# Kernel tuning notes

Hardware: AMD Instinct MI355X
Metric: run time of the kernel (lower is better)

The kernel has to match this reference:

```python
import jax, jax.numpy as jnp
import numpy as np
import math

B, NO, T, NM, P = 16, 64, 21, 768, 20
CA, CM, D, H, L, K = 29, 9, 256, 8, 6, 16
N = NO + NM
HD = D // H


def _linrelu(x, w, b):
    return jax.nn.relu(x @ w.T + b)


def _layernorm(x, g, b):
    m = x.mean(-1, keepdims=True)
    v = ((x - m) ** 2).mean(-1, keepdims=True)
    return (x - m) / jnp.sqrt(v + 1e-5) * g + b


def _sine_embed(pos_xy, d):
    # MTR gen_sineembed_for_position: per-coordinate sin/cos, concat(y, x)
    half = d // 2
    dim_t = 10000.0 ** (2.0 * (jnp.arange(half) // 2).astype(jnp.float32) / half)
    scale = 2.0 * math.pi
    def interleave(e):
        return jnp.stack([jnp.sin(e[..., 0::2]), jnp.cos(e[..., 1::2])], axis=-1).reshape(e.shape)
    ex = pos_xy[..., 0:1] * scale / dim_t
    ey = pos_xy[..., 1:2] * scale / dim_t
    return jnp.concatenate([interleave(ey), interleave(ex)], axis=-1)


def _pointnet(poly, mask, pre, mid, out1, out2):
    # PointNetPolylineEncoder: pre-MLP, masked max-pool, concat pooled, MLP, masked max-pool, out-MLP
    m = mask[..., None].astype(poly.dtype)
    f = poly
    for w, b in pre:
        f = _linrelu(f, w, b)
    f = f * m  # zero invalid points (== scatter into zeros)
    pooled = f.max(axis=2)
    f = jnp.concatenate([f, jnp.broadcast_to(pooled[:, :, None, :], f.shape)], axis=-1)
    for w, b in mid:
        f = _linrelu(f, w, b)
    f = f * m
    f = f.max(axis=2)  # [B, num_poly, hidden]
    h = _linrelu(f, out1[0], out1[1])
    h = h @ out2[0].T + out2[1]
    valid = mask.any(-1)
    return jnp.where(valid[..., None], h, 0.0)


def _forward(obj_trajs, map_polylines, obj_trajs_last_pos, map_polylines_center,
             a_pre_w, a_pre_b, a_mlp_w1, a_mlp_b1, a_mlp_w2, a_mlp_b2,
             a_out_w1, a_out_b1, a_out_w2, a_out_b2,
             m_pre_w1, m_pre_b1, m_pre_w2, m_pre_b2, m_pre_w3, m_pre_b3,
             m_mlp_w1, m_mlp_b1, m_mlp_w2, m_mlp_b2,
             m_out_w1, m_out_b1, m_out_w2, m_out_b2,
             attn_wqkv, attn_bqkv, attn_wo, attn_bo,
             ffn_w1, ffn_b1, ffn_w2, ffn_b2,
             ln1_g, ln1_b, ln2_g, ln2_b,
             obj_trajs_mask, map_polylines_mask):
    obj_in = jnp.concatenate([obj_trajs, obj_trajs_mask[..., None].astype(obj_trajs.dtype)], axis=-1)
    obj_feat = _pointnet(obj_in, obj_trajs_mask, [(a_pre_w, a_pre_b)],
                         [(a_mlp_w1, a_mlp_b1), (a_mlp_w2, a_mlp_b2)],
                         (a_out_w1, a_out_b1), (a_out_w2, a_out_b2))
    map_feat = _pointnet(map_polylines, map_polylines_mask,
                         [(m_pre_w1, m_pre_b1), (m_pre_w2, m_pre_b2), (m_pre_w3, m_pre_b3)],
                         [(m_mlp_w1, m_mlp_b1), (m_mlp_w2, m_mlp_b2)],
                         (m_out_w1, m_out_b1), (m_out_w2, m_out_b2))
    x = jnp.concatenate([obj_feat, map_feat], axis=1)                      # [B, N, D]
    pos = jnp.concatenate([obj_trajs_last_pos, map_polylines_center], axis=1)  # [B, N, 3]
    # KNN neighbor graph within each batch element (all tokens valid)
    d2 = jnp.sum((pos[:, :, None, :] - pos[:, None, :, :]) ** 2, axis=-1)  # [B, N, N]
    _, idx = jax.lax.top_k(-d2, K)                                          # [B, N, K]
    pe = _sine_embed(pos[..., :2], D)                                       # [B, N, D]
    scaling = HD ** -0.5
    gather = jax.vmap(lambda a, i: a[i])  # per-batch neighbor gather
    out = x
    for l in range(L):  # post-norm transformer encoder layers with local (KNN) attention
        qk_in = out + pe
        wq, wk, wv = attn_wqkv[l, :D], attn_wqkv[l, D:2 * D], attn_wqkv[l, 2 * D:]
        bq, bk, bv = attn_bqkv[l, :D], attn_bqkv[l, D:2 * D], attn_bqkv[l, 2 * D:]
        q = ((qk_in @ wq.T + bq) * scaling).reshape(B, N, H, HD)
        k = (qk_in @ wk.T + bk).reshape(B, N, H, HD)
        v = (out @ wv.T + bv).reshape(B, N, H, HD)
        kg = gather(k, idx)  # [B, N, K, H, HD]
        vg = gather(v, idx)
        attn = jax.nn.softmax(jnp.einsum('bnhd,bnkhd->bnhk', q, kg), axis=-1)
        o = jnp.einsum('bnhk,bnkhd->bnhd', attn, vg).reshape(B, N, D)
        o = o @ attn_wo[l].T + attn_bo[l]
        h = _layernorm(out + o, ln1_g[l], ln1_b[l])
        ff = jax.nn.relu(h @ ffn_w1[l].T + ffn_b1[l]) @ ffn_w2[l].T + ffn_b2[l]
        out = _layernorm(h + ff, ln2_g[l], ln2_b[l])
    return out  # global_token_feature [B, N, D]


def setup_inputs():
    ks = iter(jax.random.split(jax.random.key(0), 64))
    def rn(shape, s=1.0):
        return jax.random.normal(next(ks), shape, dtype=jnp.float32) * s
    w = 0.02
    inp = {
        'obj_trajs': rn((B, NO, T, CA)),
        'map_polylines': rn((B, NM, P, CM)),
        'obj_trajs_last_pos': rn((B, NO, 3)),
        'map_polylines_center': rn((B, NM, 3)),
        'a_pre_w': rn((D, CA + 1), w), 'a_pre_b': rn((D,), w),
        'a_mlp_w1': rn((D, 2 * D), w), 'a_mlp_b1': rn((D,), w),
        'a_mlp_w2': rn((D, D), w), 'a_mlp_b2': rn((D,), w),
        'a_out_w1': rn((D, D), w), 'a_out_b1': rn((D,), w),
        'a_out_w2': rn((D, D), w), 'a_out_b2': rn((D,), w),
        'm_pre_w1': rn((64, CM), w), 'm_pre_b1': rn((64,), w),
        'm_pre_w2': rn((64, 64), w), 'm_pre_b2': rn((64,), w),
        'm_pre_w3': rn((64, 64), w), 'm_pre_b3': rn((64,), w),
        'm_mlp_w1': rn((64, 128), w), 'm_mlp_b1': rn((64,), w),
        'm_mlp_w2': rn((64, 64), w), 'm_mlp_b2': rn((64,), w),
        'm_out_w1': rn((64, 64), w), 'm_out_b1': rn((64,), w),
        'm_out_w2': rn((D, 64), w), 'm_out_b2': rn((D,), w),
        'attn_wqkv': rn((L, 3 * D, D), w), 'attn_bqkv': rn((L, 3 * D), w),
        'attn_wo': rn((L, D, D), w), 'attn_bo': rn((L, D), w),
        'ffn_w1': rn((L, 4 * D, D), w), 'ffn_b1': rn((L, 4 * D), w),
        'ffn_w2': rn((L, D, 4 * D), w), 'ffn_b2': rn((L, D), w),
        'ln1_g': jnp.ones((L, D), jnp.float32), 'ln1_b': jnp.zeros((L, D), jnp.float32),
        'ln2_g': jnp.ones((L, D), jnp.float32), 'ln2_b': jnp.zeros((L, D), jnp.float32),
        'obj_trajs_mask': jnp.ones((B, NO, T), bool),
        'map_polylines_mask': jnp.ones((B, NM, P), bool),
        'track_index_to_predict': jax.random.randint(next(ks), (B,), 0, NO),
    }
    return inp


def reference(obj_trajs, map_polylines, obj_trajs_last_pos, map_polylines_center,
              a_pre_w, a_pre_b, a_mlp_w1, a_mlp_b1, a_mlp_w2, a_mlp_b2,
              a_out_w1, a_out_b1, a_out_w2, a_out_b2,
              m_pre_w1, m_pre_b1, m_pre_w2, m_pre_b2, m_pre_w3, m_pre_b3,
              m_mlp_w1, m_mlp_b1, m_mlp_w2, m_mlp_b2,
              m_out_w1, m_out_b1, m_out_w2, m_out_b2,
              attn_wqkv, attn_bqkv, attn_wo, attn_bo,
              ffn_w1, ffn_b1, ffn_w2, ffn_b2,
              ln1_g, ln1_b, ln2_g, ln2_b,
              obj_trajs_mask, map_polylines_mask, track_index_to_predict):
    # track_index_to_predict only selects rows of the output downstream; core encoder output returned
    return _forward(obj_trajs, map_polylines, obj_trajs_last_pos, map_polylines_center,
                    a_pre_w, a_pre_b, a_mlp_w1, a_mlp_b1, a_mlp_w2, a_mlp_b2,
                    a_out_w1, a_out_b1, a_out_w2, a_out_b2,
                    m_pre_w1, m_pre_b1, m_pre_w2, m_pre_b2, m_pre_w3, m_pre_b3,
                    m_mlp_w1, m_mlp_b1, m_mlp_w2, m_mlp_b2,
                    m_out_w1, m_out_b1, m_out_w2, m_out_b2,
                    attn_wqkv, attn_bqkv, attn_wo, attn_bo,
                    ffn_w1, ffn_b1, ffn_w2, ffn_b2,
                    ln1_g, ln1_b, ln2_g, ln2_b,
                    obj_trajs_mask, map_polylines_mask)
```

## Files before the change

kernel.cpp:

```cpp
#include <hip/hip_runtime.h>
#include <hip/hip_bf16.h>

typedef unsigned short u16;
typedef _Float16 h16;

#define BB 16
#define NO 64
#define TT 21
#define NM 768
#define PP 20
#define CAx 29
#define CMx 9
#define DD 256
#define HH 8
#define LL 6
#define KK 16
#define NN (NO + NM)
#define HDX (DD / HH)
#define MTOT (BB * NN)
#define MAPR (BB * NM * PP)

typedef __attribute__((ext_vector_type(8))) h16 h8v;
typedef __attribute__((ext_vector_type(4))) h16 h4v;
typedef __attribute__((ext_vector_type(4))) float f4v;
// ... 209 lines not shown
                GLOAD_LDS16(&W[(size_t)(n0 + r + lrow) * K + k0 + lcol], &WS[r][0]);
            }
        }
        __syncthreads();
        h8v af[WM];
        #pragma unroll
        for (int mi = 0; mi < WM; mi++)
            af[mi] = *(const h8v*)&AS[wr * (WM * 16) + mi * 16 + fr][rdo];
        #pragma unroll
        for (int nj = 0; nj < 4; nj++) {
            h8v bf = *(const h8v*)&WS[wc * 64 + nj * 16 + fr][rdo];
            #pragma unroll
            for (int mi = 0; mi < WM; mi++)
                acc[mi][nj] = __builtin_amdgcn_mfma_f32_16x16x32_f16(af[mi], bf, acc[mi][nj], 0, 0, 0);
        }
    }
    #pragma unroll
    for (int mi = 0; mi < WM; mi++) {
        #pragma unroll
        for (int nj = 0; nj < 4; nj++) {
            int col = n0 + wc * 64 + nj * 16 + fr;
            float bb = bias ? bias[col] : 0.f;
            #pragma unroll
            for (int r = 0; r < 4; r++) {
                int row = m0 + wr * (WM * 16) + mi * 16 + (lane >> 4) * 4 + r;
                float v = acc[mi][nj][r] + bb;
                if (addrow) v += addrow[(size_t)(row / ardiv) * arld + col];
                if (RELU) v = fmaxf(v, 0.f);
                if (F16OUT) {
                    C16[(size_t)row * ldc + col] = (h16)v;
                } else {
                    int drow = row;
                    if (ROWMAP) drow = row + rm_add + (row / rm_div) * rm_mul;
                    Cf[(size_t)drow * ldc + col] = v;
                }
            }
        }
    }
}

__global__ __launch_bounds__(256) void split_x0(
    const float* __restrict__ X, const h16* __restrict__ PE16,
    h16* __restrict__ X16, h16* __restrict__ XP16)
{
    size_t base = ((size_t)blockIdx.x * 256 + threadIdx.x) * 4;
    float4 x = *(const float4*)&X[base];
    h4v pe = *(const h4v*)&PE16[base];
    h4v a, b;
    a.x = (h16)x.x; a.y = (h16)x.y; a.z = (h16)x.z; a.w = (h16)x.w;
    b.x = (h16)(x.x + (float)pe.x); b.y = (h16)(x.y + (float)pe.y);
    b.z = (h16)(x.z + (float)pe.z); b.w = (h16)(x.w + (float)pe.w);
    *(h4v*)&X16[base] = a;
    *(h4v*)&XP16[base] = b;
}

__global__ __launch_bounds__(256) void fused_map3(
    const h16* __restrict__ A,
    const h16* __restrict__ W1,
    const h16* __restrict__ W2, const h16* __restrict__ W3,
    const float* __restrict__ b1, const float* __restrict__ b2, const float* __restrict__ b3,
    h16* __restrict__ Out)
{
    __shared__ __align__(16) h16 AS[128][32];
    __shared__ __align__(16) h16 G0[2][128][32];
    __shared__ __align__(16) h16 G1[2][128][32];
    __shared__ __align__(16) h16 W1S[64][32];
    __shared__ __align__(16) h16 W2S[2][64][32];
    __shared__ __align__(16) h16 W3S[2][64][32];
    const int m0 = blockIdx.x * 128;
    const int tid = threadIdx.x;
    const int wave = tid >> 6, lane = tid & 63;
    const int fr = lane & 15, kb = lane >> 4;
    const int lrow = lane >> 2, lcol = SWZ_LCOL(lane);
    const int rdo = SWZ_RD(kb, fr);

    #pragma unroll
    for (int q = 0; q < 2; q++)
        GLOAD_LDS16(&A[(size_t)(m0 + wave * 32 + q * 16 + lrow) * 32 + lcol],
                    &AS[wave * 32 + q * 16][0]);
    GLOAD_LDS16(&W1[(size_t)(wave * 16 + lrow) * 32 + lcol], &W1S[wave * 16][0]);
    #pragma unroll
    for (int t = 0; t < 2; t++) {
        GLOAD_LDS16(&W2[(size_t)(wave * 16 + lrow) * 64 + t * 32 + lcol], &W2S[t][wave * 16][0]);
        GLOAD_LDS16(&W3[(size_t)(wave * 16 + lrow) * 64 + t * 32 + lcol], &W3S[t][wave * 16][0]);
    }
    __syncthreads();
    #pragma unroll
    for (int mi = 0; mi < 2; mi++) {
        h8v af = *(const h8v*)&AS[wave * 32 + mi * 16 + fr][rdo];
        #pragma unroll
        for (int nj = 0; nj < 4; nj++) {
            f4v a = {0.f, 0.f, 0.f, 0.f};
            h8v bf = *(const h8v*)&W1S[nj * 16 + fr][rdo];
            a = __builtin_amdgcn_mfma_f32_16x16x32_f16(af, bf, a, 0, 0, 0);
            int col = nj * 16 + fr, ch = col >> 5, kl = col & 31;
            float bb = b1[col];
            #pragma unroll
            for (int r = 0; r < 4; r++) {
                int row = wave * 32 + mi * 16 + kb * 4 + r;
                G0[ch][row][SWZ_ELEM(row, kl)] = (h16)fmaxf(a[r] + bb, 0.f);
            }
        }
    }
    __syncthreads();
    #pragma unroll
    for (int mi = 0; mi < 2; mi++) {
        #pragma unroll
        for (int nj = 0; nj < 4; nj++) {
            f4v a = {0.f, 0.f, 0.f, 0.f};
            #pragma unroll
            for (int t = 0; t < 2; t++) {
                h8v af = *(const h8v*)&G0[t][wave * 32 + mi * 16 + fr][rdo];
                h8v bf = *(const h8v*)&W2S[t][nj * 16 + fr][rdo];
                a = __builtin_amdgcn_mfma_f32_16x16x32_f16(af, bf, a, 0, 0, 0);
            }
            int col = nj * 16 + fr, ch = col >> 5, kl = col & 31;
            float bb = b2[col];
            #pragma unroll
            for (int r = 0; r < 4; r++) {
                int row = wave * 32 + mi * 16 + kb * 4 + r;
                G1[ch][row][SWZ_ELEM(row, kl)] = (h16)fmaxf(a[r] + bb, 0.f);
            }
        }
    }
    __syncthreads();
    #pragma unroll
    for (int mi = 0; mi < 2; mi++) {
        #pragma unroll
        for (int nj = 0; nj < 4; nj++) {
            f4v a = {0.f, 0.f, 0.f, 0.f};
            #pragma unroll
            for (int t = 0; t < 2; t++) {
                h8v af = *(const h8v*)&G1[t][wave * 32 + mi * 16 + fr][rdo];
                h8v bf = *(const h8v*)&W3S[t][nj * 16 + fr][rdo];
                a = __builtin_amdgcn_mfma_f32_16x16x32_f16(af, bf, a, 0, 0, 0);
            }
            int col = nj * 16 + fr;
            float bb = b3[col];
            #pragma unroll
            for (int r = 0; r < 4; r++) {
                int row = m0 + wave * 32 + mi * 16 + kb * 4 + r;
                Out[(size_t)row * 64 + col] = (h16)fmaxf(a[r] + bb, 0.f);
            }
        }
    }
}

__global__ __launch_bounds__(256) void fused_map2(
    const h16* __restrict__ A,
    const h16* __restrict__ W1,
    const h16* __restrict__ W2,
    const float* __restrict__ b2,
    const float* __restrict__ pooled,
    h16* __restrict__ Out)
{
    __shared__ __align__(16) h16 AS[2][128][32];
    __shared__ __align__(16) h16 G0[2][128][32];
    __shared__ __align__(16) h16 W1S[2][64][32];
    __shared__ __align__(16) h16 W2S[2][64][32];
    const int m0 = blockIdx.x * 128;
    const int tid = threadIdx.x;
    const int wave = tid >> 6, lane = tid & 63;
    const int fr = lane & 15, kb = lane >> 4;
    const int lrow = lane >> 2, lcol = SWZ_LCOL(lane);
    const int rdo = SWZ_RD(kb, fr);

    #pragma unroll
    for (int t = 0; t < 2; t++) {
        #pragma unroll
        for (int q = 0; q < 2; q++)
            GLOAD_LDS16(&A[(size_t)(m0 + wave * 32 + q * 16 + lrow) * 64 + t * 32 + lcol],
                        &AS[t][wave * 32 + q * 16][0]);
        GLOAD_LDS16(&W1[(size_t)(wave * 16 + lrow) * 64 + t * 32 + lcol], &W1S[t][wave * 16][0]);
        GLOAD_LDS16(&W2[(size_t)(wave * 16 + lrow) * 64 + t * 32 + lcol], &W2S[t][wave * 16][0]);
    }
    __syncthreads();
    #pragma unroll
    for (int mi = 0; mi < 2; mi++) {
        #pragma unroll
        for (int nj = 0; nj < 4; nj++) {
            f4v a = {0.f, 0.f, 0.f, 0.f};
            #pragma unroll
            for (int t = 0; t < 2; t++) {
                h8v af = *(const h8v*)&AS[t][wave * 32 + mi * 16 + fr][rdo];
                h8v bf = *(const h8v*)&W1S[t][nj * 16 + fr][rdo];
                a = __builtin_amdgcn_mfma_f32_16x16x32_f16(af, bf, a, 0, 0, 0);
            }
            int col = nj * 16 + fr, ch = col >> 5, kl = col & 31;
            #pragma unroll
            for (int r = 0; r < 4; r++) {
                int row = wave * 32 + mi * 16 + kb * 4 + r;
                int grow = m0 + row;
                float v = a[r] + pooled[(size_t)(grow / PP) * 64 + col];
                G0[ch][row][SWZ_ELEM(row, kl)] = (h16)fmaxf(v, 0.f);
            }
        }
    }
    __syncthreads();
    #pragma unroll
    for (int mi = 0; mi < 2; mi++) {
        #pragma unroll
        for (int nj = 0; nj < 4; nj++) {
            f4v a = {0.f, 0.f, 0.f, 0.f};
            #pragma unroll
            for (int t = 0; t < 2; t++) {
                h8v af = *(const h8v*)&G0[t][wave * 32 + mi * 16 + fr][rdo];
                h8v bf = *(const h8v*)&W2S[t][nj * 16 + fr][rdo];
                a = __builtin_amdgcn_mfma_f32_16x16x32_f16(af, bf, a, 0, 0, 0);
            }
            int col = nj * 16 + fr;
            float bb = b2[col];
            #pragma unroll
            for (int r = 0; r < 4; r++) {
                int row = m0 + wave * 32 + mi * 16 + kb * 4 + r;
                Out[(size_t)row * 64 + col] = (h16)fmaxf(a[r] + bb, 0.f);
            }
        }
    }
}

template<bool RELU, bool F16OUT>
__global__ __launch_bounds__(256) void gemm_mfma(
    const h16* __restrict__ A, const h16* __restrict__ A2, int a2min,
    const h16* __restrict__ W, const float* __restrict__ bias,
    float* __restrict__ Cf, h16* __restrict__ C16,
    int K, int ldc, int coff, float scale, int scale_until)
{
    __shared__ __align__(16) h16 AS[128][32];
    __shared__ __align__(16) h16 WS[128][32];
    const int m0 = blockIdx.x * 128;
    const int n0 = blockIdx.y * 128;
    const h16* pA = (n0 >= a2min) ? A2 : A;
    const int tid = threadIdx.x;
    const int wave = tid >> 6, lane = tid & 63;
    const int wr = wave >> 1, wc = wave & 1;
    const int fr = lane & 15, kb = lane >> 4;
    const int lrow = lane >> 2;
    const int lcol = SWZ_LCOL(lane);
    const int rdo = SWZ_RD(kb, fr);

    f4v acc[4][4];
    #pragma unroll
    for (int i = 0; i < 4; i++)
        #pragma unroll
        for (int j = 0; j < 4; j++) { f4v z = {0.f, 0.f, 0.f, 0.f}; acc[i][j] = z; }

    for (int k0 = 0; k0 < K; k0 += 32) {
        __syncthreads();
        #pragma unroll
        for (int i = 0; i < 2; i++) {
            const int r = wave * 32 + i * 16;
            const size_t grow = (size_t)(r + lrow);
            GLOAD_LDS16(&pA[(m0 + grow) * K + k0 + lcol], &AS[r][0]);
            GLOAD_LDS16(&W [(n0 + grow) * K + k0 + lcol], &WS[r][0]);
        }
        __syncthreads();
        h8v af[4];
        #pragma unroll
        for (int mi = 0; mi < 4; mi++)
            af[mi] = *(const h8v*)&AS[wr * 64 + mi * 16 + fr][rdo];
        #pragma unroll
        for (int nj = 0; nj < 4; nj++) {
            h8v bf = *(const h8v*)&WS[wc * 64 + nj * 16 + fr][rdo];
            #pragma unroll
            for (int mi = 0; mi < 4; mi++)
                acc[mi][nj] = __builtin_amdgcn_mfma_f32_16x16x32_f16(af[mi], bf, acc[mi][nj], 0, 0, 0);
        }
    }
    #pragma unroll
    for (int mi = 0; mi < 4; mi++) {
        #pragma unroll
        for (int nj = 0; nj < 4; nj++) {
            int col = n0 + wc * 64 + nj * 16 + fr;
            float bb = bias[col];
            #pragma unroll
            for (int r = 0; r < 4; r++) {
                int row = m0 + wr * 64 + mi * 16 + (lane >> 4) * 4 + r;
                float v = acc[mi][nj][r] + bb;
                if (RELU) v = fmaxf(v, 0.f);
                int gcol = coff + col;
                if (gcol < scale_until) v *= scale;
                if (F16OUT) {
                    C16[(size_t)row * ldc + gcol] = (h16)v;
                } else {
                    Cf[(size_t)row * ldc + gcol] = v;
                }
            }
        }
    }
}

template<int PEMODE>
__global__ __launch_bounds__(512) void fused_layer(
    const h16* __restrict__ AO16, const h16* __restrict__ Wo,
    const float* __restrict__ bo, const h16* __restrict__ X16r,
    const float* __restrict__ g1, const float* __restrict__ bt1,
    const h16* __restrict__ W1,
    const h16* __restrict__ W2,
    const float* __restrict__ b1, const float* __restrict__ b2,
    const float* __restrict__ g2, const float* __restrict__ bt2,
    float* __restrict__ OutF, h16* __restrict__ O16,
    const h16* __restrict__ PE16p, h16* __restrict__ P16)
{
    __shared__ __align__(16) h16 AOS[8][32][32];
    __shared__ __align__(16) h16 HS[8][32][32];
    __shared__ __align__(16) h16 GS[2][32][32];
    __shared__ __align__(16) h16 WSu[16384];
    __shared__ float red_s[2][8][32];
    const int m0 = blockIdx.x * 32;
    const int tid = threadIdx.x;
    const int wave = tid >> 6, lane = tid & 63;
    const int fr = lane & 15, kb = lane >> 4;
    const int lrow = lane >> 2, lcol = SWZ_LCOL(lane);
    const int rdo = SWZ_RD(kb, fr);
    const int mi1 = wave >> 2, nj1 = wave & 3;

    #pragma unroll
    for (int q = 0; q < 2; q++)
        GLOAD_LDS16(&AO16[(size_t)(m0 + q * 16 + lrow) * 256 + wave * 32 + lcol],
                    &AOS[wave][q * 16][0]);

    float xo[4][4];
    float rsum1[4] = {0.f, 0.f, 0.f, 0.f}, rsq1[4] = {0.f, 0.f, 0.f, 0.f};
    #pragma unroll
    for (int oc = 0; oc < 4; oc++) {
        __syncthreads();
        #pragma unroll
        for (int q = 0; q < 4; q++)
            GLOAD_LDS16(&Wo[(size_t)(oc * 64 + q * 16 + lrow) * 256 + wave * 32 + lcol],
                        &WSu[wave * 2048 + (q * 16) * 32]);
        __syncthreads();
        f4v o1 = {0.f, 0.f, 0.f, 0.f};
        #pragma unroll
        for (int t = 0; t < 8; t++) {
            h8v af = *(const h8v*)&AOS[t][mi1 * 16 + fr][rdo];
            h8v bf = *(const h8v*)&WSu[t * 2048 + (nj1 * 16 + fr) * 32 + rdo];
            o1 = __builtin_amdgcn_mfma_f32_16x16x32_f16(af, bf, o1, 0, 0, 0);
        }
        int col = oc * 64 + nj1 * 16 + fr;
        float bb = bo[col];
        #pragma unroll
        for (int r = 0; r < 4; r++) {
            int row = mi1 * 16 + kb * 4 + r;
            float v = o1[r] + bb + (float)X16r[(size_t)(m0 + row) * 256 + col];
            xo[oc][r] = v;
            rsum1[r] += v;
            rsq1[r] += v * v;
        }
    }
    #pragma unroll
    for (int off = 1; off < 16; off <<= 1)
        #pragma unroll
        for (int r = 0; r < 4; r++) {
            rsum1[r] += __shfl_xor(rsum1[r], off);
            rsq1[r]  += __shfl_xor(rsq1[r], off);
        }
    if (fr == 0) {
        #pragma unroll
        for (int r = 0; r < 4; r++) {
            red_s[0][wave][mi1 * 16 + kb * 4 + r] = rsum1[r];
            red_s[1][wave][mi1 * 16 + kb * 4 + r] = rsq1[r];
        }
    } else if (fr == 1) {
        #pragma unroll
        for (int r = 0; r < 4; r++) {
            red_s[0][wave][(1 - mi1) * 16 + kb * 4 + r] = 0.f;
            red_s[1][wave][(1 - mi1) * 16 + kb * 4 + r] = 0.f;
        }
    }
    __syncthreads();
    float mean1[4], inv1[4];
    #pragma unroll
    for (int r = 0; r < 4; r++) {
        int rid = mi1 * 16 + kb * 4 + r;
        float s = 0.f, sq = 0.f;
        #pragma unroll
        for (int w = 0; w < 8; w++) { s += red_s[0][w][rid]; sq += red_s[1][w][rid]; }
        mean1[r] = s * (1.f / 256.f);
        float var = sq * (1.f / 256.f) - mean1[r] * mean1[r];
        inv1[r] = rsqrtf(var + 1e-5f);
    }
    #pragma unroll
    for (int oc = 0; oc < 4; oc++) {
        int col = oc * 64 + nj1 * 16 + fr;
        int ch = col >> 5, kl = col & 31;
        float gg = g1[col], bb = bt1[col];
        #pragma unroll
        for (int r = 0; r < 4; r++) {
            int row = mi1 * 16 + kb * 4 + r;
            float h = (xo[oc][r] - mean1[r]) * inv1[r] * gg + bb;
            HS[ch][row][SWZ_ELEM(row, kl)] = (h16)h;
        }
    }
    __syncthreads();

    f4v acc2[2][2];
    #pragma unroll
    for (int i = 0; i < 2; i++)
        #pragma unroll
        for (int j = 0; j < 2; j++) { f4v z = {0.f, 0.f, 0.f, 0.f}; acc2[i][j] = z; }

    for (int c = 0; c < 16; c++) {
        const int H0 = c * 64;
        __syncthreads();
        #pragma unroll
        for (int q = 0; q < 4; q++)
            GLOAD_LDS16(&W1[(size_t)(H0 + q * 16 + lrow) * 256 + wave * 32 + lcol],
                        &WSu[wave * 2048 + (q * 16) * 32]);
        __syncthreads();
        f4v a1 = {0.f, 0.f, 0.f, 0.f};
        #pragma unroll
        for (int t = 0; t < 8; t++) {
            h8v af = *(const h8v*)&HS[t][mi1 * 16 + fr][rdo];
            h8v bf = *(const h8v*)&WSu[t * 2048 + (nj1 * 16 + fr) * 32 + rdo];
            a1 = __builtin_amdgcn_mfma_f32_16x16x32_f16(af, bf, a1, 0, 0, 0);
        }
        {
            int col = nj1 * 16 + fr, ch = col >> 5, kl = col & 31;
            float bb = b1[H0 + col];
            #pragma unroll
            for (int r = 0; r < 4; r++) {
                int row = mi1 * 16 + kb * 4 + r;
                GS[ch][row][SWZ_ELEM(row, kl)] = (h16)fmaxf(a1[r] + bb, 0.f);
            }
        }
        __syncthreads();
        #pragma unroll
        for (int t2 = 0; t2 < 2; t2++)
            #pragma unroll
            for (int q = 0; q < 2; q++)
                GLOAD_LDS16(&W2[(size_t)(wave * 32 + q * 16 + lrow) * 1024 + H0 + t2 * 32 + lcol],
                            &WSu[t2 * 8192 + (wave * 32 + q * 16) * 32]);
        __syncthreads();
        #pragma unroll
        for (int t2 = 0; t2 < 2; t2++) {
            #pragma unroll
            for (int mi = 0; mi < 2; mi++) {
                h8v af = *(const h8v*)&GS[t2][mi * 16 + fr][rdo];
                #pragma unroll
                for (int nj = 0; nj < 2; nj++) {
                    h8v bf = *(const h8v*)&WSu[t2 * 8192 + (wave * 32 + nj * 16 + fr) * 32 + rdo];
                    acc2[mi][nj] = __builtin_amdgcn_mfma_f32_16x16x32_f16(af, bf, acc2[mi][nj], 0, 0, 0);
                }
            }
        }
    }
    float x[2][2][4];
    float rsum[2][4], rsq[2][4];
    #pragma unroll
    for (int mi = 0; mi < 2; mi++)
        #pragma unroll
        for (int r = 0; r < 4; r++) { rsum[mi][r] = 0.f; rsq[mi][r] = 0.f; }
    #pragma unroll
    for (int mi = 0; mi < 2; mi++) {
        #pragma unroll
        for (int nj = 0; nj < 2; nj++) {
            int col = wave * 32 + nj * 16 + fr;
            int ch = col >> 5, kl = col & 31;
            float bb = b2[col];
            #pragma unroll
            for (int r = 0; r < 4; r++) {
                int row = mi * 16 + kb * 4 + r;
                float res = (float)HS[ch][row][SWZ_ELEM(row, kl)];
                float v = acc2[mi][nj][r] + bb + res;
                x[mi][nj][r] = v;
                rsum[mi][r] += v;
                rsq[mi][r] += v * v;
            }
        }
    }
    #pragma unroll
    for (int off = 1; off < 16; off <<= 1) {
        #pragma unroll
        for (int mi = 0; mi < 2; mi++)
            #pragma unroll
            for (int r = 0; r < 4; r++) {
                rsum[mi][r] += __shfl_xor(rsum[mi][r], off);
                rsq[mi][r]  += __shfl_xor(rsq[mi][r], off);
            }
    }
    __syncthreads();
    if (fr == 0) {
        #pragma unroll
        for (int mi = 0; mi < 2; mi++)
            #pragma unroll
            for (int r = 0; r < 4; r++) {
                int rid = mi * 16 + kb * 4 + r;
                red_s[0][wave][rid] = rsum[mi][r];
                red_s[1][wave][rid] = rsq[mi][r];
            }
    }
    __syncthreads();
    #pragma unroll
    for (int mi = 0; mi < 2; mi++) {
        #pragma unroll
        for (int r = 0; r < 4; r++) {
            int rid = mi * 16 + kb * 4 + r;
            float s = 0.f, sq = 0.f;
            #pragma unroll
            for (int w = 0; w < 8; w++) { s += red_s[0][w][rid]; sq += red_s[1][w][rid]; }
            float mean = s * (1.f / 256.f);
            float var = sq * (1.f / 256.f) - mean * mean;
            float inv = rsqrtf(var + 1e-5f);
            #pragma unroll
            for (int nj = 0; nj < 2; nj++) {
                int col = wave * 32 + nj * 16 + fr;
                float o = (x[mi][nj][r] - mean) * inv * g2[col] + bt2[col];
                size_t idx = (size_t)(m0 + rid) * 256 + col;
                if (PEMODE == 2) {
                    OutF[idx] = o;
                } else {
                    O16[idx] = (h16)o;
                    P16[idx] = (h16)(o + (float)PE16p[idx]);
                }
            }
        }
    }
}

__global__ __launch_bounds__(256) void attn_kernel(
    const h16* __restrict__ QKV16, const int* __restrict__ IDX,
    h16* __restrict__ AO16)
{
    __shared__ __align__(16) h16 Ks[32][256];
    __shared__ float p_s[2][HH][16];
    __shared__ int gid_s[2][16];
    const int sub = threadIdx.x >> 7;
    const int t = threadIdx.x & 127;
    const int wave = threadIdx.x >> 6, lane = threadIdx.x & 63;
    const int xcd = blockIdx.x & 7;
    const int j = blockIdx.x >> 3;
    const int b = (j / 416) * 8 + xcd;
    const int row = b * NN + (j % 416) * 2 + sub;
    const int h = t >> 4, k = t & 15;
    int nb = IDX[(size_t)row * 16 + k];
    int g = b * NN + nb;
    if (h == 0) gid_s[sub][k] = g;
    __syncthreads();
    #pragma unroll
    for (int i = 0; i < 4; i++) {
        int s0 = wave * 8 + i * 2;
        int s = s0 + (lane >> 5);
        int gs = gid_s[s >> 4][s & 15];
        int clog = (lane & 31) ^ (s & 7);
        GLOAD_LDS16(&QKV16[(size_t)gs * 768 + 256 + clog * 8], &Ks[s0][0]);
    }
    __syncthreads();
    const h16* q = &QKV16[(size_t)row * 768 + h * HDX];
    const int sidx = sub * 16 + k;
    float s = 0.f;
    #pragma unroll
    for (int c = 0; c < 4; c++) {
        h8v q8 = *(const h8v*)&q[c * 8];
        h8v k8 = *(const h8v*)&Ks[sidx][(((h * 4 + c) ^ (sidx & 7)) * 8)];
        #pragma unroll
        for (int e = 0; e < 8; e++) s += (float)q8[e] * (float)k8[e];
    }
    float m = s;
    #pragma unroll
    for (int off = 8; off; off >>= 1) m = fmaxf(m, __shfl_xor(m, off, 16));
    float e = expf(s - m);
    float sum = e;
    #pragma unroll
    for (int off = 8; off; off >>= 1) sum += __shfl_xor(sum, off, 16);
    p_s[sub][h][k] = e / sum;
    __syncthreads();
    const int d0 = t * 2;
    const int hh = d0 >> 5, dd = d0 & 31;
    float o0 = 0.f, o1 = 0.f;
    #pragma unroll
    for (int kk = 0; kk < 16; kk++) {
        int gg = gid_s[sub][kk];
        const h16* vr = &QKV16[(size_t)gg * 768 + 512 + hh * HDX + dd];
        float p = p_s[sub][hh][kk];
        o0 += p * (float)vr[0];
        o1 += p * (float)vr[1];
    }
    size_t base = (size_t)row * DD + d0;
    AO16[base] = (h16)o0;
    AO16[base + 1] = (h16)o1;
}

extern "C" void kernel_launch(void* const* d_in, const int* in_sizes, int n_in,
                              void* d_out, int out_size, void* d_ws, size_t ws_size,
                              hipStream_t stream)
{
    const float* obj      = (const float*)d_in[0];
    const float* mp       = (const float*)d_in[1];
    const float* opos     = (const float*)d_in[2];
    const float* mpos     = (const float*)d_in[3];
    const float* a_pre_w  = (const float*)d_in[4];
    const float* a_pre_b  = (const float*)d_in[5];
    const float* a_mlp_w1 = (const float*)d_in[6];
    const float* a_mlp_b1 = (const float*)d_in[7];
    const float* a_mlp_w2 = (const float*)d_in[8];
    const float* a_mlp_b2 = (const float*)d_in[9];
    const float* a_out_w1 = (const float*)d_in[10];
    const float* a_out_b1 = (const float*)d_in[11];
    const float* a_out_w2 = (const float*)d_in[12];
    const float* a_out_b2 = (const float*)d_in[13];
    const float* m_pre_w1 = (const float*)d_in[14];
    const float* m_pre_b1 = (const float*)d_in[15];
    const float* m_pre_w2 = (const float*)d_in[16];
    const float* m_pre_b2 = (const float*)d_in[17];
    const float* m_pre_w3 = (const float*)d_in[18];
    const float* m_pre_b3 = (const float*)d_in[19];
    const float* m_mlp_w1 = (const float*)d_in[20];
    const float* m_mlp_b1 = (const float*)d_in[21];
    const float* m_mlp_w2 = (const float*)d_in[22];
    const float* m_mlp_b2 = (const float*)d_in[23];
    const float* m_out_w1 = (const float*)d_in[24];
    const float* m_out_b1 = (const float*)d_in[25];
    const float* m_out_w2 = (const float*)d_in[26];
    const float* m_out_b2 = (const float*)d_in[27];
    const float* attn_wqkv = (const float*)d_in[28];
    const float* attn_bqkv = (const float*)d_in[29];
    const float* attn_wo   = (const float*)d_in[30];
    const float* attn_bo   = (const float*)d_in[31];
    const float* ffn_w1    = (const float*)d_in[32];
    const float* ffn_b1    = (const float*)d_in[33];
    const float* ffn_w2    = (const float*)d_in[34];
    const float* ffn_b2    = (const float*)d_in[35];
    const float* ln1_g     = (const float*)d_in[36];
    const float* ln1_b     = (const float*)d_in[37];
    const float* ln2_g     = (const float*)d_in[38];
    const float* ln2_b     = (const float*)d_in[39];

    const size_t M = MTOT;
    float* ws   = (float*)d_ws;
    float* X    = ws;
    float* PEr  = X   + M * 256;
    float* QKVr = PEr + M * 256;
    float* Hpad = QKVr + M * 768;
    h16* AO16   = (h16*)(Hpad + M * 256);
    h16* X16    = AO16 + M * 256;
    h16* XP16   = X16  + M * 256;
    h16* H16    = XP16 + M * 256;
    h16* whf    = H16  + M * 256;
    h16* wpnf   = whf  + 4718592;
    int* IDX    = (int*)(wpnf + WPN_TOT);

    h16* PE16 = (h16*)PEr;
    h16* QKV16 = (h16*)QKVr;

    h16* PN0f = (h16*)QKVr;
    h16* PN1f = PN0f + 15728640;
    h16* SB   = PN0f + 31457280;
    h16* PLf  = SB;
    h16* GMf  = SB + 786432;
    h16* HVf  = SB + 1572864;
    h16* APLf = SB + 2359296;
    h16* AGMf = SB + 2621440;
    h16* AHVf = SB + 2883584;
    float* PCf = (float*)(SB + 3145728);
    float* APC = PCf + 786432;

    knn_kernel<<<BB * 208, 256, 0, stream>>>(opos, mpos, IDX);
    prep_all<<<PRB_TOT, 256, 0, stream>>>(
        mp, obj, opos, mpos,
        attn_wqkv, attn_wo, ffn_w1, ffn_w2,
        m_pre_w1, m_pre_w2, m_pre_w3, m_mlp_w1, m_mlp_w2, m_out_w1, m_out_w2,
        a_pre_w, a_mlp_w1, a_mlp_w2, a_out_w1, a_out_w2,
        PN0f , PN1f , PE16, wpnf, whf);

    {
        h16* PA32 = PN1f;
        h16* PB   = PN0f + 7864320;
        h16* PA2  = PN1f;
        gemm_pn<128, true, true, false><<<dim3(168, 2), 256, 0, stream>>>(
            PA32, wpnf + APW_O, a_pre_b, nullptr, 1, 0,
            nullptr, PB, 32, 256, 1, 0, 0);
        pool_max8<21><<<128, 256, 0, stream>>>(PB, APLf, 8);
        gemm_pn<128, false, false, false><<<dim3(8, 2), 256, 0, stream>>>(
            APLf, wpnf + AW1B_O, a_mlp_b1, nullptr, 1, 0,
            APC, nullptr, 256, 256, 1, 0, 0);
        gemm_pn<128, true, true, false><<<dim3(168, 2), 256, 0, stream>>>(
            PB, wpnf + AW1A_O, nullptr, APC, 21, 256,
            nullptr, PA2, 256, 256, 1, 0, 0);
        gemm_pn<128, true, true, false><<<dim3(168, 2), 256, 0, stream>>>(
            PA2, wpnf + AW2S_O, a_mlp_b2, nullptr, 1, 0,
            nullptr, PB, 256, 256, 1, 0, 0);
        pool_max8<21><<<128, 256, 0, stream>>>(PB, AGMf, 8);
        gemm_pn<128, true, true, false><<<dim3(8, 2), 256, 0, stream>>>(
            AGMf, wpnf + AOW1_O, a_out_b1, nullptr, 1, 0,
            nullptr, AHVf, 256, 256, 1, 0, 0);
        gemm_pn<128, false, false, true><<<dim3(8, 2), 256, 0, stream>>>(
            AHVf, wpnf + AOW2_O, a_out_b2, nullptr, 1, 0,
            X, nullptr, 256, 256, 64, 768, 0);
    }

    {
        fused_map3<<<MAPR / 128, 256, 0, stream>>>(
            PN0f, wpnf + W1P_O, wpnf + W2S_O, wpnf + W3S_O,
            m_pre_b1, m_pre_b2, m_pre_b3, PN1f);
        pool_max8<20><<<384, 256, 0, stream>>>(PN1f, PLf, 6);
        gemm_pn<64, false, false, false><<<dim3(96, 1), 256, 0, stream>>>(
            PLf, wpnf + MW1B_O, m_mlp_b1, nullptr, 1, 0,
            PCf, nullptr, 64, 64, 1, 0, 0);
        fused_map2<<<MAPR / 128, 256, 0, stream>>>(
            PN1f, wpnf + MW1A_O, wpnf + MW2S_O,
            m_mlp_b2, PCf, PN0f);
        pool_max8<20><<<384, 256, 0, stream>>>(PN0f, GMf, 6);
        gemm_pn<64, true, true, false><<<dim3(96, 1), 256, 0, stream>>>(
            GMf, wpnf + OW1S_O, m_out_b1, nullptr, 1, 0,
            nullptr, HVf, 64, 64, 1, 0, 0);
        gemm_pn<128, false, false, true><<<dim3(96, 2), 256, 0, stream>>>(
            HVf, wpnf + OW2S_O, m_out_b2, nullptr, 1, 0,
            X, nullptr, 64, 256, 768, 64, 64);
    }

    split_x0<<<(int)(M * 256 / 1024), 256, 0, stream>>>(X, PE16, X16, XP16);

    const float scal = 0.17677669529663687f;
    const int MB = MTOT / 128;
    for (int l = 0; l < LL; l++) {
        const size_t wb = (size_t)l * 786432;
        const h16* wqkv_f = whf + wb;
        const h16* wo_f   = whf + wb + 196608;
        const h16* f1_f   = whf + wb + 262144;
        const h16* f2_f   = whf + wb + 524288;
        const float* bqkv = attn_bqkv + (size_t)l * 768;
        gemm_mfma<false, true><<<dim3(MB, 6), 256, 0, stream>>>(
            XP16, X16, 512, wqkv_f, bqkv,
            nullptr, QKV16, 256, 768, 0, scal, 256);
        attn_kernel<<<MTOT / 2, 256, 0, stream>>>(QKV16, IDX, AO16);
        if (l == LL - 1) {
            fused_layer<2><<<MTOT / 32, 512, 0, stream>>>(
                AO16, wo_f, attn_bo + (size_t)l * 256, X16,
                ln1_g + l * 256, ln1_b + l * 256,
                f1_f, f2_f, ffn_b1 + (size_t)l * 1024, ffn_b2 + (size_t)l * 256,
                ln2_g + l * 256, ln2_b + l * 256,
                (float*)d_out, nullptr, nullptr, nullptr);
        } else {
            fused_layer<1><<<MTOT / 32, 512, 0, stream>>>(
                AO16, wo_f, attn_bo + (size_t)l * 256, X16,
                ln1_g + l * 256, ln1_b + l * 256,
                f1_f, f2_f, ffn_b1 + (size_t)l * 1024, ffn_b2 + (size_t)l * 256,
                ln2_g + l * 256, ln2_b + l * 256,
                nullptr, X16, PE16, XP16);
        }
    }
}
```

Measured before the change: 688.6 us.

## Double fused layer row tile to 64 and widen per-wave output tiles

The fused out-projection + LN + FFN + LN kernel now processes 64 rows per block instead of 32. Waves are rearranged into a 4x2 grid, each computing a 16-row by 64/128-column tile with A fragments held in registers. The larger tile halves how often each block reloads weight tiles (Wo, W1, W2) per row, which cuts weight traffic and barrier count per row. In exchange it uses roughly double the LDS and more registers, and launches half as many blocks, which may lower occupancy.

Result: no change. 682.0 us (-1.0%).

```diff
diff --git a/kernel.cpp b/kernel.cpp
--- a/kernel.cpp
+++ b/kernel.cpp
@@ -535,50 +535,56 @@
     float* __restrict__ OutF, h16* __restrict__ O16,
     const h16* __restrict__ PE16p, h16* __restrict__ P16)
 {
-    __shared__ __align__(16) h16 AOS[8][32][32];
-    __shared__ __align__(16) h16 HS[8][32][32];
-    __shared__ __align__(16) h16 GS[2][32][32];
-    __shared__ __align__(16) h16 WSu[16384];
-    __shared__ float red_s[2][8][32];
-    const int m0 = blockIdx.x * 32;
+    __shared__ __align__(16) h16 AOS[8][64][32];
+    __shared__ __align__(16) h16 HS[8][64][32];
+    __shared__ __align__(16) h16 GS[4][64][32];
+    __shared__ __align__(16) h16 WSu[32768];
+    __shared__ float red_s[2][8][64];
+    const int m0 = blockIdx.x * 64;
     const int tid = threadIdx.x;
     const int wave = tid >> 6, lane = tid & 63;
+    const int wr = wave >> 1, wc = wave & 1;
     const int fr = lane & 15, kb = lane >> 4;
     const int lrow = lane >> 2, lcol = SWZ_LCOL(lane);
     const int rdo = SWZ_RD(kb, fr);
-    const int mi1 = wave >> 2, nj1 = wave & 3;
-
-    #pragma unroll
-    for (int q = 0; q < 2; q++)
+
+    #pragma unroll
+    for (int q = 0; q < 4; q++)
         GLOAD_LDS16(&AO16[(size_t)(m0 + q * 16 + lrow) * 256 + wave * 32 + lcol],
                     &AOS[wave][q * 16][0]);
 
-    float xo[4][4];
+    float xo[2][4][4];
     float rsum1[4] = {0.f, 0.f, 0.f, 0.f}, rsq1[4] = {0.f, 0.f, 0.f, 0.f};
     #pragma unroll
-    for (int oc = 0; oc < 4; oc++) {
+    for (int oc = 0; oc < 2; oc++) {
         __syncthreads();
         #pragma unroll
-        for (int q = 0; q < 4; q++)
-            GLOAD_LDS16(&Wo[(size_t)(oc * 64 + q * 16 + lrow) * 256 + wave * 32 + lcol],
-                        &WSu[wave * 2048 + (q * 16) * 32]);
+        for (int q = 0; q < 8; q++)
+            GLOAD_LDS16(&Wo[(size_t)(oc * 128 + q * 16 + lrow) * 256 + wave * 32 + lcol],
+                        &WSu[wave * 4096 + (q * 16) * 32]);
         __syncthreads();
-        f4v o1 = {0.f, 0.f, 0.f, 0.f};
-        #pragma unroll
-        for (int t = 0; t < 8; t++) {
-            h8v af = *(const h8v*)&AOS[t][mi1 * 16 + fr][rdo];
-            h8v bf = *(const h8v*)&WSu[t * 2048 + (nj1 * 16 + fr) * 32 + rdo];
-            o1 = __builtin_amdgcn_mfma_f32_16x16x32_f16(af, bf, o1, 0, 0, 0);
-        }
-        int col = oc * 64 + nj1 * 16 + fr;
-        float bb = bo[col];
-        #pragma unroll
-        for (int r = 0; r < 4; r++) {
-            int row = mi1 * 16 + kb * 4 + r;
-            float v = o1[r] + bb + (float)X16r[(size_t)(m0 + row) * 256 + col];
-            xo[oc][r] = v;
-            rsum1[r] += v;
-            rsq1[r] += v * v;
+        h8v aof[8];
+        #pragma unroll
+        for (int t = 0; t < 8; t++)
+            aof[t] = *(const h8v*)&AOS[t][wr * 16 + fr][rdo];
+        #pragma unroll
+        for (int nj = 0; nj < 4; nj++) {
+            f4v o1 = {0.f, 0.f, 0.f, 0.f};
+            #pragma unroll
+            for (int t = 0; t < 8; t++) {
+                h8v bf = *(const h8v*)&WSu[t * 4096 + (wc * 64 + nj * 16 + fr) * 32 + rdo];
+                o1 = __builtin_amdgcn_mfma_f32_16x16x32_f16(aof[t], bf, o1, 0, 0, 0);
+            }
+            int col = oc * 128 + wc * 64 + nj * 16 + fr;
+            float bb = bo[col];
+            #pragma unroll
+            for (int r = 0; r < 4; r++) {
+                int row = wr * 16 + kb * 4 + r;
+                float v = o1[r] + bb + (float)X16r[(size_t)(m0 + row) * 256 + col];
+                xo[oc][nj][r] = v;
+                rsum1[r] += v;
+                rsq1[r] += v * v;
+            }
         }
     }
     #pragma unroll
@@ -588,24 +594,19 @@
             rsum1[r] += __shfl_xor(rsum1[r], off);
             rsq1[r]  += __shfl_xor(rsq1[r], off);
         }
-    if (fr == 0) {
+    if (fr < 4) {
+        int grp = (wr + fr) & 3;
         #pragma unroll
         for (int r = 0; r < 4; r++) {
-            red_s[0][wave][mi1 * 16 + kb * 4 + r] = rsum1[r];
-            red_s[1][wave][mi1 * 16 + kb * 4 + r] = rsq1[r];
-        }
-    } else if (fr == 1) {
-        #pragma unroll
-        for (int r = 0; r < 4; r++) {
-            red_s[0][wave][(1 - mi1) * 16 + kb * 4 + r] = 0.f;
-            red_s[1][wave][(1 - mi1) * 16 + kb * 4 + r] = 0.f;
+            red_s[0][wave][grp * 16 + kb * 4 + r] = (fr == 0) ? rsum1[r] : 0.f;
+            red_s[1][wave][grp * 16 + kb * 4 + r] = (fr == 0) ? rsq1[r] : 0.f;
         }
     }
     __syncthreads();
     float mean1[4], inv1[4];
     #pragma unroll
     for (int r = 0; r < 4; r++) {
-        int rid = mi1 * 16 + kb * 4 + r;
+        int rid = wr * 16 + kb * 4 + r;
         float s = 0.f, sq = 0.f;
         #pragma unroll
         for (int w = 0; w < 8; w++) { s += red_s[0][w][rid]; sq += red_s[1][w][rid]; }
@@ -614,138 +615,126 @@
         inv1[r] = rsqrtf(var + 1e-5f);
     }
     #pragma unroll
-    for (int oc = 0; oc < 4; oc++) {
-        int col = oc * 64 + nj1 * 16 + fr;
-        int ch = col >> 5, kl = col & 31;
-        float gg = g1[col], bb = bt1[col];
-        #pragma unroll
-        for (int r = 0; r < 4; r++) {
-            int row = mi1 * 16 + kb * 4 + r;
-            float h = (xo[oc][r] - mean1[r]) * inv1[r] * gg + bb;
-            HS[ch][row][SWZ_ELEM(row, kl)] = (h16)h;
-        }
-    }
-    __syncthreads();
-
-    f4v acc2[2][2];
-    #pragma unroll
-    for (int i = 0; i < 2; i++)
-        #pragma unroll
-        for (int j = 0; j < 2; j++) { f4v z = {0.f, 0.f, 0.f, 0.f}; acc2[i][j] = z; }
-
-    for (int c = 0; c < 16; c++) {
-        const int H0 = c * 64;
+    for (int oc = 0; oc < 2; oc++)
+        #pragma unroll
+        for (int nj = 0; nj < 4; nj++) {
+            int col = oc * 128 + wc * 64 + nj * 16 + fr;
+            int ch = col >> 5, kl = col & 31;
+            float gg = g1[col], bb = bt1[col];
+            #pragma unroll
+            for (int r = 0; r < 4; r++) {
+                int row = wr * 16 + kb * 4 + r;
+                float h = (xo[oc][nj][r] - mean1[r]) * inv1[r] * gg + bb;
+                HS[ch][row][SWZ_ELEM(row, kl)] = (h16)h;
+            }
+        }
+    __syncthreads();
+
+    h8v haf[8];
+    #pragma unroll
+    for (int t = 0; t < 8; t++)
+        haf[t] = *(const h8v*)&HS[t][wr * 16 + fr][rdo];
+
+    f4v acc2[8];
+    #pragma unroll
+    for (int j = 0; j < 8; j++) { f4v z = {0.f, 0.f, 0.f, 0.f}; acc2[j] = z; }
+
+    for (int c = 0; c < 8; c++) {
+        const int H0 = c * 128;
         __syncthreads();
         #pragma unroll
-        for (int q = 0; q < 4; q++)
+        for (int q = 0; q < 8; q++)
             GLOAD_LDS16(&W1[(size_t)(H0 + q * 16 + lrow) * 256 + wave * 32 + lcol],
-                        &WSu[wave * 2048 + (q * 16) * 32]);
+                        &WSu[wave * 4096 + (q * 16) * 32]);
         __syncthreads();
-        f4v a1 = {0.f, 0.f, 0.f, 0.f};
-        #pragma unroll
-        for (int t = 0; t < 8; t++) {
-            h8v af = *(const h8v*)&HS[t][mi1 * 16 + fr][rdo];
-            h8v bf = *(const h8v*)&WSu[t * 2048 + (nj1 * 16 + fr) * 32 + rdo];
-            a1 = __builtin_amdgcn_mfma_f32_16x16x32_f16(af, bf, a1, 0, 0, 0);
-        }
-        {
-            int col = nj1 * 16 + fr, ch = col >> 5, kl = col & 31;
-            float bb = b1[H0 + col];
+        #pragma unroll
+        for (int nj = 0; nj < 4; nj++) {
+            f4v a1 = {0.f, 0.f, 0.f, 0.f};
+            #pragma unroll
+            for (int t = 0; t < 8; t++) {
+                h8v bf = *(const h8v*)&WSu[t * 4096 + (wc * 64 + nj * 16 + fr) * 32 + rdo];
+                a1 = __builtin_amdgcn_mfma_f32_16x16x32_f16(haf[t], bf, a1, 0, 0, 0);
+            }
+            int n = wc * 64 + nj * 16 + fr;
+            int ch = n >> 5, kl = n & 31;
+            float bb = b1[H0 + n];
             #pragma unroll
             for (int r = 0; r < 4; r++) {
-                int row = mi1 * 16 + kb * 4 + r;
+                int row = wr * 16 + kb * 4 + r;
                 GS[ch][row][SWZ_ELEM(row, kl)] = (h16)fmaxf(a1[r] + bb, 0.f);
             }
         }
         __syncthreads();
         #pragma unroll
-        for (int t2 = 0; t2 < 2; t2++)
+        for (int t2 = 0; t2 < 4; t2++)
             #pragma unroll
             for (int q = 0; q < 2; q++)
                 GLOAD_LDS16(&W2[(size_t)(wave * 32 + q * 16 + lrow) * 1024 + H0 + t2 * 32 + lcol],
                             &WSu[t2 * 8192 + (wave * 32 + q * 16) * 32]);
         __syncthreads();
         #pragma unroll
-        for (int t2 = 0; t2 < 2; t2++) {
-            #pragma unroll
-            for (int mi = 0; mi < 2; mi++) {
-                h8v af = *(const h8v*)&GS[t2][mi * 16 + fr][rdo];
-                #pragma unroll
-                for (int nj = 0; nj < 2; nj++) {
-                    h8v bf = *(const h8v*)&WSu[t2 * 8192 + (wave * 32 + nj * 16 + fr) * 32 + rdo];
-                    acc2[mi][nj] = __builtin_amdgcn_mfma_f32_16x16x32_f16(af, bf, acc2[mi][nj], 0, 0, 0);
-                }
-            }
-        }
-    }
-    float x[2][2][4];
-    float rsum[2][4], rsq[2][4];
-    #pragma unroll
-    for (int mi = 0; mi < 2; mi++)
-        #pragma unroll
-        for (int r = 0; r < 4; r++) { rsum[mi][r] = 0.f; rsq[mi][r] = 0.f; }
-    #pragma unroll
-    for (int mi = 0; mi < 2; mi++) {
-        #pragma unroll
-        for (int nj = 0; nj < 2; nj++) {
-            int col = wave * 32 + nj * 16 + fr;
-            int ch = col >> 5, kl = col & 31;
-            float bb = b2[col];
-            #pragma unroll
-            for (int r = 0; r < 4; r++) {
-                int row = mi * 16 + kb * 4 + r;
-                float res = (float)HS[ch][row][SWZ_ELEM(row, kl)];
-                float v = acc2[mi][nj][r] + bb + res;
-                x[mi][nj][r] = v;
-                rsum[mi][r] += v;
-                rsq[mi][r] += v * v;
-            }
-        }
-    }
-    #pragma unroll
-    for (int off = 1; off < 16; off <<= 1) {
-        #pragma unroll
-        for (int mi = 0; mi < 2; mi++)
-            #pragma unroll
-            for (int r = 0; r < 4; r++) {
-                rsum[mi][r] += __shfl_xor(rsum[mi][r], off);
-                rsq[mi][r]  += __shfl_xor(rsq[mi][r], off);
-            }
-    }
-    __syncthreads();
-    if (fr == 0) {
-        #pragma unroll
-        for (int mi = 0; mi < 2; mi++)
-            #pragma unroll
-            for (int r = 0; r < 4; r++) {
-                int rid = mi * 16 + kb * 4 + r;
-                red_s[0][wave][rid] = rsum[mi][r];
-                red_s[1][wave][rid] = rsq[mi][r];
-            }
-    }
-    __syncthreads();
-    #pragma unroll
-    for (int mi = 0; mi < 2; mi++) {
+        for (int t2 = 0; t2 < 4; t2++) {
+            h8v gaf = *(const h8v*)&GS[t2][wr * 16 + fr][rdo];
+            #pragma unroll
+            for (int nj = 0; nj < 8; nj++) {
+                h8v bf = *(const h8v*)&WSu[t2 * 8192 + (wc * 128 + nj * 16 + fr) * 32 + rdo];
+                acc2[nj] = __builtin_amdgcn_mfma_f32_16x16x32_f16(gaf, bf, acc2[nj], 0, 0, 0);
+            }
+        }
+    }
+    float x[8][4];
+    float rsum[4] = {0.f, 0.f, 0.f, 0.f}, rsq[4] = {0.f, 0.f, 0.f, 0.f};
+    #pragma unroll
+    for (int nj = 0; nj < 8; nj++) {
+        int col = wc * 128 + nj * 16 + fr;
+        int ch = col >> 5, kl = col & 31;
+        float bb = b2[col];
         #pragma unroll
         for (int r = 0; r < 4; r++) {
-            int rid = mi * 16 + kb * 4 + r;
-            float s = 0.f, sq = 0.f;
-            #pragma unroll
-            for (int w = 0; w < 8; w++) { s += red_s[0][w][rid]; sq += red_s[1][w][rid]; }
-            float mean = s * (1.f / 256.f);
-            float var = sq * (1.f / 256.f) - mean * mean;
-            float inv = rsqrtf(var + 1e-5f);
-            #pragma unroll
-            for (int nj = 0; nj < 2; nj++) {
-                int col = wave * 32 + nj * 16 + fr;
-                float o = (x[mi][nj][r] - mean) * inv * g2[col] + bt2[col];
-                size_t idx = (size_t)(m0 + rid) * 256 + col;
-                if (PEMODE == 2) {
-                    OutF[idx] = o;
-                } else {
-                    O16[idx] = (h16)o;
-                    P16[idx] = (h16)(o + (float)PE16p[idx]);
-                }
+            int row = wr * 16 + kb * 4 + r;
+            float res = (float)HS[ch][row][SWZ_ELEM(row, kl)];
+            float v = acc2[nj][r] + bb + res;
+            x[nj][r] = v;
+            rsum[r] += v;
+            rsq[r] += v * v;
+        }
+    }
+    #pragma unroll
+    for (int off = 1; off < 16; off <<= 1)
+        #pragma unroll
+        for (int r = 0; r < 4; r++) {
+            rsum[r] += __shfl_xor(rsum[r], off);
+            rsq[r]  += __shfl_xor(rsq[r], off);
+        }
+    __syncthreads();
+    if (fr < 4) {
+        int grp = (wr + fr) & 3;
+        #pragma unroll
+        for (int r = 0; r < 4; r++) {
+            red_s[0][wave][grp * 16 + kb * 4 + r] = (fr == 0) ? rsum[r] : 0.f;
+            red_s[1][wave][grp * 16 + kb * 4 + r] = (fr == 0) ? rsq[r] : 0.f;
+        }
+    }
+    __syncthreads();
+    #pragma unroll
+    for (int r = 0; r < 4; r++) {
+        int rid = wr * 16 + kb * 4 + r;
+        float s = 0.f, sq = 0.f;
+        #pragma unroll
+        for (int w = 0; w < 8; w++) { s += red_s[0][w][rid]; sq += red_s[1][w][rid]; }
+        float mean = s * (1.f / 256.f);
+        float var = sq * (1.f / 256.f) - mean * mean;
+        float inv = rsqrtf(var + 1e-5f);
+        #pragma unroll
+        for (int nj = 0; nj < 8; nj++) {
+            int col = wc * 128 + nj * 16 + fr;
+            float o = (x[nj][r] - mean) * inv * g2[col] + bt2[col];
+            size_t idx = (size_t)(m0 + rid) * 256 + col;
+            if (PEMODE == 2) {
+                OutF[idx] = o;
+            } else {
+                O16[idx] = (h16)o;
+                P16[idx] = (h16)(o + (float)PE16p[idx]);
             }
         }
     }
@@ -958,14 +947,14 @@
             nullptr, QKV16, 256, 768, 0, scal, 256);
         attn_kernel<<<MTOT / 2, 256, 0, stream>>>(QKV16, IDX, AO16);
         if (l == LL - 1) {
-            fused_layer<2><<<MTOT / 32, 512, 0, stream>>>(
+            fused_layer<2><<<MTOT / 64, 512, 0, stream>>>(
                 AO16, wo_f, attn_bo + (size_t)l * 256, X16,
                 ln1_g + l * 256, ln1_b + l * 256,
                 f1_f, f2_f, ffn_b1 + (size_t)l * 1024, ffn_b2 + (size_t)l * 256,
                 ln2_g + l * 256, ln2_b + l * 256,
                 (float*)d_out, nullptr, nullptr, nullptr);
         } else {
-            fused_layer<1><<<MTOT / 32, 512, 0, stream>>>(
+            fused_layer<1><<<MTOT / 64, 512, 0, stream>>>(
                 AO16, wo_f, attn_bo + (size_t)l * 256, X16,
                 ln1_g + l * 256, ln1_b + l * 256,
                 f1_f, f2_f, ffn_b1 + (size_t)l * 1024, ffn_b2 + (size_t)l * 256,
```
